# Optimization experiments

Hardware: AMD Instinct MI355X
Metric: run time of the kernel (lower is better)

## Reference

```python
import jax, jax.numpy as jnp
import numpy as np

B, T, V = 512, 200, 2048
E, H, I, A = 20, 100, 64, 32  # embedding, hidden, intermediate, actions


def setup_inputs() -> dict:
    key = jax.random.key(0)
    ks = jax.random.split(key, 12)
    batch = jax.random.uniform(ks[0], (B, T, V), dtype=jnp.float32)
    lengths = jax.random.randint(ks[1], (B,), 1, T + 1)
    s = 0.05
    W_emb = jax.random.normal(ks[2], (E, V), dtype=jnp.float32) * s
    b_emb = jnp.zeros((E,), jnp.float32)
    W_ih = jax.random.normal(ks[3], (4 * H, E), dtype=jnp.float32) * s
    W_hh = jax.random.normal(ks[4], (4 * H, H), dtype=jnp.float32) * s
    b_ih = jnp.zeros((4 * H,), jnp.float32)
    # torch init sets forget-gate bias (second quarter) to 1.0 in bias_hh
    b_hh = jnp.zeros((4 * H,), jnp.float32).at[H:2 * H].set(1.0)
    W1 = jax.random.normal(ks[5], (I, H), dtype=jnp.float32) * s
    b1 = jnp.zeros((I,), jnp.float32)
    W2 = jax.random.normal(ks[6], (A, I), dtype=jnp.float32) * s
    b2 = jnp.zeros((A,), jnp.float32)
    h0 = jnp.zeros((B, H), jnp.float32)
    c0 = jnp.zeros((B, H), jnp.float32)
    return {"batch": batch, "lengths": lengths, "W_emb": W_emb, "b_emb": b_emb,
            "W_ih": W_ih, "W_hh": W_hh, "b_ih": b_ih, "b_hh": b_hh,
            "W1": W1, "b1": b1, "W2": W2, "b2": b2, "h0": h0, "c0": c0}


def reference(batch, lengths, W_emb, b_emb, W_ih, W_hh, b_ih, b_hh,
              W1, b1, W2, b2, h0, c0):
    # Embedding via Linear: [B,T,V] @ [V,E] -> [B,T,E]
    emb = jnp.einsum('btv,ev->bte', batch, W_emb) + b_emb
    # Precompute input contribution to all gates: [B,T,4H]
    xg = jnp.einsum('bte,ge->btg', emb, W_ih) + b_ih + b_hh

    def step(carry, xg_t):
        h, c = carry
        gates = xg_t + h @ W_hh.T  # [B,4H]
        i, f, g, o = jnp.split(gates, 4, axis=-1)  # torch gate order i,f,g,o
        c = jax.nn.sigmoid(f) * c + jax.nn.sigmoid(i) * jnp.tanh(g)
        h = jax.nn.sigmoid(o) * jnp.tanh(c)
        return (h, c), h

    _, ys = jax.lax.scan(step, (h0, c0), jnp.swapaxes(xg, 0, 1))  # ys: [T,B,H]
    nb = batch.shape[0]
    h_final = ys[lengths - 1, jnp.arange(nb)]  # [B,H] output at last valid step
    inter = jax.nn.relu(h_final @ W1.T + b1)
    actions = inter @ W2.T + b2
    return actions
```

## Files before the change

### kernel.cpp

```cpp
#include <hip/hip_runtime.h>

#define BB 512
#define TT 200
#define VV 2048
#define EE 20
#define HH 100
#define G4 400
#define II 64
#define AA 32
#define NT 25
#define NCHUNK 64

typedef _Float16 half8 __attribute__((ext_vector_type(8)));
typedef float    f32x4 __attribute__((ext_vector_type(4)));

#define WS_BF_OFF    1024
#define WS_WIHF_OFF  (WS_BF_OFF + 32768)
#define WS_WHHF_OFF  (WS_WIHF_OFF + 6400)
#define WS_BIASC_OFF (WS_WHHF_OFF + 25600)
#define WS_EMB_OFF   (WS_BIASC_OFF + 400)
#define WS_XG_OFF    (WS_EMB_OFF + 2048000)

__global__ __launch_bounds__(512) void k0_prep(
    const int* __restrict__ lengths, const float* __restrict__ W_emb,
    const float* __restrict__ W_ih, const float* __restrict__ W_hh,
    const float* __restrict__ b_ih, const float* __restrict__ b_hh,
    int* __restrict__ off, _Float16* __restrict__ Bfrag,
    _Float16* __restrict__ Wihf, _Float16* __restrict__ Whhf,
    float* __restrict__ biasc)
{
    if (blockIdx.x == 0) {
        __shared__ int s[BB];
        int tid = threadIdx.x;
        s[tid] = lengths[tid];
        __syncthreads();
        for (int d = 1; d < BB; d <<= 1) {
            int v = (tid >= d) ? s[tid - d] : 0;
            __syncthreads();
            if (tid >= d) s[tid] += v;
            __syncthreads();
        }
        off[tid + 1] = s[tid];
        if (tid == 0) off[0] = 0;
        return;
    }
    int F = (blockIdx.x - 1) * 512 + threadIdx.x;
    if (F < 65536) {
        int e = F & 7, l = (F >> 3) & 63, nn = (F >> 9) & 1, c = F >> 10;
        int k = c * 32 + (l >> 4) * 8 + e;
        int col = nn * 16 + (l & 15);
        float v = (col < EE) ? W_emb[(size_t)col * VV + k] : 0.f;
        Bfrag[F] = (_Float16)v;
        return;
    }
    F -= 65536;
    if (F < 12800) {
        int e = F & 7, l = (F >> 3) & 63, nt = F >> 9;
        int rp = nt * 16 + (l & 15);
        int j = rp >> 2, g = rp & 3;
        int k = 8 * (l >> 4) + e;
        float v = (k < EE) ? W_ih[(size_t)(g * HH + j) * EE + k] : 0.f;
        Wihf[F] = (_Float16)v;
        return;
    }
    F -= 12800;
    if (F < 51200) {
        int e = F & 7, l = (F >> 3) & 63, c = (F >> 9) & 3, m = F >> 11;
        int rp = m * 16 + (l & 15);
        int j = rp >> 2, g = rp & 3;
        int k = 32 * c + 8 * (l >> 4) + e;
        float v = (k < HH) ? W_hh[(size_t)(g * HH + j) * HH + k] : 0.f;
        Whhf[F] = (_Float16)v;
        return;
    }
    F -= 51200;
    if (F < 400) {
        int j = F >> 2, g = F & 3;
        biasc[F] = b_ih[g * HH + j] + b_hh[g * HH + j];
    }
}

__global__ __launch_bounds__(256) void k1_embed(
    const float* __restrict__ batch, const int* __restrict__ off,
    const _Float16* __restrict__ Bfrag, const float* __restrict__ b_emb,
    float* __restrict__ emb)
{
    const int Nv = off[BB];
    if (blockIdx.x * 64 >= Nv) return;

    const int lane  = threadIdx.x & 63;
    const int wid   = threadIdx.x >> 6;
    const int rbase = blockIdx.x * 64 + wid * 16;

    int lrow = rbase + (lane & 15);
    int lr = (lrow < Nv) ? lrow : (Nv - 1);
    int lo = 0, hi = BB;
    while (lo + 1 < hi) {
        int mid = (lo + hi) >> 1;
        if (off[mid] <= lr) lo = mid; else hi = mid;
    }
    const int lroff = lo * TT + (lr - off[lo]);

    const float* __restrict__ aptr = batch + (size_t)lroff * VV + ((lane >> 4) * 8);
    const half8* __restrict__ bptr = reinterpret_cast<const half8*>(Bfrag) + lane;

    f32x4 acc0 = {0.f, 0.f, 0.f, 0.f};
    f32x4 acc1 = {0.f, 0.f, 0.f, 0.f};

#pragma unroll 4
    for (int c = 0; c < NCHUNK; ++c) {
        float4 a0 = *reinterpret_cast<const float4*>(aptr + c * 32);
        float4 a1 = *reinterpret_cast<const float4*>(aptr + c * 32 + 4);
        half8 b0 = bptr[(c * 2 + 0) * 64];
        half8 b1 = bptr[(c * 2 + 1) * 64];
        half8 av;
        av[0] = (_Float16)a0.x; av[1] = (_Float16)a0.y;
        av[2] = (_Float16)a0.z; av[3] = (_Float16)a0.w;
        av[4] = (_Float16)a1.x; av[5] = (_Float16)a1.y;
        av[6] = (_Float16)a1.z; av[7] = (_Float16)a1.w;
        acc0 = __builtin_amdgcn_mfma_f32_16x16x32_f16(av, b0, acc0, 0, 0, 0);
        acc1 = __builtin_amdgcn_mfma_f32_16x16x32_f16(av, b1, acc1, 0, 0, 0);
    }

    const int col0 = lane & 15;
    const float bias0 = b_emb[col0];
    const float bias1 = (col0 < 4) ? b_emb[16 + col0] : 0.f;
#pragma unroll
    for (int r = 0; r < 4; ++r) {
        int srow = rbase + (lane >> 4) * 4 + r;
        if (srow < Nv) {
            emb[(size_t)srow * EE + col0] = acc0[r] + bias0;
            if (col0 < 4)
                emb[(size_t)srow * EE + 16 + col0] = acc1[r] + bias1;
        }
    }
}

__global__ __launch_bounds__(256, 2) void k1_xg(
    const float* __restrict__ emb, const int* __restrict__ off,
    const _Float16* __restrict__ Wihf, const float* __restrict__ biasc,
    float* __restrict__ xg)
{
    __shared__ __align__(16) uint4 wl[NT * 64];
    __shared__ float bl[G4];

    const int tid = threadIdx.x;
    const int Nv = off[BB];
    for (int i = tid; i < NT * 64; i += 256) wl[i] = reinterpret_cast<const uint4*>(Wihf)[i];
    for (int i = tid; i < G4; i += 256) bl[i] = biasc[i];
    __syncthreads();

    const int lane = tid & 63, wid = tid >> 6;
    const int T = blockIdx.x * 4 + wid;
    if (T * 16 >= Nv) return;

    const int lr = min(T * 16 + (lane & 15), Nv - 1);
    const int kb = (lane >> 4) * 8;
    const float* ap = emb + (size_t)lr * EE;
    float4 p0 = make_float4(0.f, 0.f, 0.f, 0.f), p1 = p0;
    if (kb < EE)     p0 = *reinterpret_cast<const float4*>(ap + kb);
    if (kb + 4 < EE) p1 = *reinterpret_cast<const float4*>(ap + kb + 4);
    half8 av;
    av[0] = (_Float16)p0.x; av[1] = (_Float16)p0.y;
    av[2] = (_Float16)p0.z; av[3] = (_Float16)p0.w;
    av[4] = (_Float16)p1.x; av[5] = (_Float16)p1.y;
    av[6] = (_Float16)p1.z; av[7] = (_Float16)p1.w;

    const int rbase = T * 16 + 4 * (lane >> 4);
    const int cl = lane & 15;
#pragma unroll
    for (int nt = 0; nt < NT; ++nt) {
        half8 bf = *reinterpret_cast<const half8*>(&wl[nt * 64 + lane]);
        f32x4 a = {0.f, 0.f, 0.f, 0.f};
        a = __builtin_amdgcn_mfma_f32_16x16x32_f16(av, bf, a, 0, 0, 0);
        float bias = bl[nt * 16 + cl];
#pragma unroll
        for (int r = 0; r < 4; ++r) {
            if (rbase + r < Nv)
                xg[(size_t)(rbase + r) * G4 + nt * 16 + cl] = a[r] + bias;
        }
    }
}

__device__ __forceinline__ float fast_sig(float x) { return 1.f / (1.f + __expf(-x)); }
__device__ __forceinline__ float fast_tanh(float x) { return 2.f * fast_sig(2.f * x) - 1.f; }

#define STEP(T_, CUR_, XC_, XN_)  do {                                                        \
    uint4 rb0_ = *reinterpret_cast<const uint4*>(&bfrag[CUR_][0][lane][0]);                   \
    uint4 rb1_ = *reinterpret_cast<const uint4*>(&bfrag[CUR_][1][lane][0]);                   \
    uint4 rb2_ = *reinterpret_cast<const uint4*>(&bfrag[CUR_][2][lane][0]);                   \
    uint4 rb3_ = *reinterpret_cast<const uint4*>(&bfrag[CUR_][3][lane][0]);                   \
    _Pragma("unroll")                                                                         \
    for (int it = 0; it < 4; ++it) if (it < ntile)                                            \
        XN_[it] = *reinterpret_cast<const float4*>(xg + rowbase + (size_t)((T_) + 1) * G4 + xgoff[it]); \
    _Pragma("unroll")                                                                         \
    for (int it = 0; it < 4; ++it) if (it < ntile) {                                          \
        f32x4 acc = __builtin_bit_cast(f32x4, XC_[it]);                                       \
        acc = __builtin_amdgcn_mfma_f32_16x16x32_f16(af[it][0], __builtin_bit_cast(half8, rb0_), acc, 0, 0, 0); \
        acc = __builtin_amdgcn_mfma_f32_16x16x32_f16(af[it][1], __builtin_bit_cast(half8, rb1_), acc, 0, 0, 0); \
        acc = __builtin_amdgcn_mfma_f32_16x16x32_f16(af[it][2], __builtin_bit_cast(half8, rb2_), acc, 0, 0, 0); \
        acc = __builtin_amdgcn_mfma_f32_16x16x32_f16(af[it][3], __builtin_bit_cast(half8, rb3_), acc, 0, 0, 0); \
        float gi = fast_sig(acc[0]);                                                          \
        float gf = fast_sig(acc[1]);                                                          \
        float gg = fast_tanh(acc[2]);                                                         \
        float go = fast_sig(acc[3]);                                                          \
        cst[it] = gf * cst[it] + gi * gg;                                                     \
        float hv = go * fast_tanh(cst[it]);                                                   \
        int j_ = jidx[it];                                                                    \
        if ((T_) == len_n - 1) hfin[n][j_] = hv;                                              \
        int kk_ = j_ & 31;                                                                    \
        _Float16* hp_ = (_Float16*)&bfrag[(CUR_) ^ 1][j_ >> 5][((kk_ >> 3) << 4) | n][(kk_ & 7) >> 1]; \
        hp_[kk_ & 1] = (_Float16)hv;                                                          \
    }                                                                                         \
    __syncthreads();                                                                          \
} while (0)

__global__ __launch_bounds__(512, 2) void k2_lstm(
    const float* __restrict__ xg, const int* __restrict__ lengths,
    const int* __restrict__ off, const _Float16* __restrict__ Whhf,
    const float* __restrict__ W1, const float* __restrict__ b1,
    const float* __restrict__ W2, const float* __restrict__ b2,
    const float* __restrict__ h0, const float* __restrict__ c0,
    float* __restrict__ out)
{
    __shared__ __align__(16) unsigned int bfrag[2][4][64][4];
    __shared__ float hfin[16][HH];
    __shared__ float inter[16][II];
    __shared__ int len_s[16], off_s[16];

    const int tid  = threadIdx.x;
    const int lane = tid & 63;
    const int w    = tid >> 6;
    const int b0   = blockIdx.x * 16;
    const int n    = lane & 15, rg = lane >> 4;

    if (tid < 16) {
        len_s[tid] = lengths[b0 + tid];
        off_s[tid] = off[b0 + tid];
    }
    for (int i = tid; i < 2 * 4 * 64 * 4; i += 512) (&bfrag[0][0][0][0])[i] = 0u;
    __syncthreads();

    int tmax = 0;
#pragma unroll
    for (int k = 0; k < 16; ++k) tmax = max(tmax, len_s[k]);

    const int ntile = (w == 7) ? 4 : 3;
    const int m0    = (w < 7) ? 3 * w : 21;
    const int len_n = len_s[n];
    const size_t rowbase = (size_t)off_s[n] * G4;

    half8 af[4][4];
    float cst[4];
    int   jidx[4], xgoff[4];
    float4 xgA[4], xgB[4];
#pragma unroll
    for (int it = 0; it < 4; ++it) if (it < ntile) {
        const int m = m0 + it;
#pragma unroll
        for (int c = 0; c < 4; ++c)
            af[it][c] = reinterpret_cast<const half8*>(Whhf)[((m * 4 + c) * 64) + lane];
        const int j = 4 * m + rg;
        jidx[it]  = j;
        xgoff[it] = 16 * m + 4 * rg;
        cst[it] = c0[(size_t)(b0 + n) * HH + j];
        float hv = h0[(size_t)(b0 + n) * HH + j];
        int kk = j & 31;
        _Float16* hp = (_Float16*)&bfrag[0][j >> 5][((kk >> 3) << 4) | n][(kk & 7) >> 1];
        hp[kk & 1] = (_Float16)hv;
        xgA[it] = *reinterpret_cast<const float4*>(xg + rowbase + xgoff[it]);
    }
    __syncthreads();

    for (int t = 0; t < tmax; t += 2) {
        STEP(t, 0, xgA, xgB);
        if (t + 1 < tmax) STEP(t + 1, 1, xgB, xgA);
    }

    for (int o = tid; o < 16 * II; o += 512) {
        int nn = o >> 6, i = o & 63;
        float a = b1[i];
        const float* w1r = W1 + i * HH;
        const float* hr  = &hfin[nn][0];
#pragma unroll
        for (int k = 0; k < HH; k += 4) {
            a += w1r[k] * hr[k] + w1r[k + 1] * hr[k + 1]
               + w1r[k + 2] * hr[k + 2] + w1r[k + 3] * hr[k + 3];
        }
        inter[nn][i] = fmaxf(a, 0.f);
    }
    __syncthreads();
    for (int o = tid; o < 16 * AA; o += 512) {
        int nn = o >> 5, ai = o & 31;
        float a = b2[ai];
        const float* w2r = W2 + ai * II;
#pragma unroll
        for (int k = 0; k < II; ++k) a += w2r[k] * inter[nn][k];
        out[(size_t)(b0 + nn) * AA + ai] = a;
    }
}

extern "C" void kernel_launch(void* const* d_in, const int* in_sizes, int n_in,
                              void* d_out, int out_size, void* d_ws, size_t ws_size,
                              hipStream_t stream) {
    const float* batch  = (const float*)d_in[0];
    const int*   lengths= (const int*)  d_in[1];
    const float* W_emb  = (const float*)d_in[2];
    const float* b_emb  = (const float*)d_in[3];
    const float* W_ih   = (const float*)d_in[4];
    const float* W_hh   = (const float*)d_in[5];
    const float* b_ih   = (const float*)d_in[6];
    const float* b_hh   = (const float*)d_in[7];
    const float* W1     = (const float*)d_in[8];
    const float* b1     = (const float*)d_in[9];
    const float* W2     = (const float*)d_in[10];
    const float* b2     = (const float*)d_in[11];
    const float* h0     = (const float*)d_in[12];
    const float* c0     = (const float*)d_in[13];
    float* out = (float*)d_out;

    int*       off   = (int*)d_ws;
    float*     wsf   = (float*)d_ws;
    _Float16*  Bfrag = (_Float16*)(wsf + WS_BF_OFF);
    _Float16*  Wihf  = (_Float16*)(wsf + WS_WIHF_OFF);
    _Float16*  Whhf  = (_Float16*)(wsf + WS_WHHF_OFF);
    float*     biasc = wsf + WS_BIASC_OFF;
    float*     emb   = wsf + WS_EMB_OFF;
    float*     xg    = wsf + WS_XG_OFF;

    k0_prep<<<255, 512, 0, stream>>>(lengths, W_emb, W_ih, W_hh, b_ih, b_hh,
                                     off, Bfrag, Wihf, Whhf, biasc);
    k1_embed<<<(BB * TT + 63) / 64, 256, 0, stream>>>(batch, off, Bfrag, b_emb, emb);
    k1_xg<<<(BB * TT / 16 + 3) / 4, 256, 0, stream>>>(emb, off, Wihf, biasc, xg);
    k2_lstm<<<BB / 16, 512, 0, stream>>>(xg, lengths, off, Whhf,
                                         W1, b1, W2, b2, h0, c0, out);
}
```

Measured before the change: 432.4 us.

## Fuse input-gate projection into LSTM recurrence and stage embeddings in shared memory

Removes the separate xg kernel and its [N,400] float intermediate. The LSTM kernel now stages fp16 embedding chunks of 16 timesteps in double-buffered shared memory and does one extra MFMA per tile for W_ih·x plus bias. This cuts global traffic and a launch, but adds MFMA work and periodic staging inside the serial recurrence loop.

```diff
diff --git a/kernel.cpp b/kernel.cpp
--- a/kernel.cpp
+++ b/kernel.cpp
@@ -19,7 +19,6 @@
 #define WS_WHHF_OFF  (WS_WIHF_OFF + 6400)
 #define WS_BIASC_OFF (WS_WHHF_OFF + 25600)
 #define WS_EMB_OFF   (WS_BIASC_OFF + 400)
-#define WS_XG_OFF    (WS_EMB_OFF + 2048000)
 
 __global__ __launch_bounds__(512) void k0_prep(
     const int* __restrict__ lengths, const float* __restrict__ W_emb,
@@ -136,66 +135,41 @@
     }
 }
 
-__global__ __launch_bounds__(256, 2) void k1_xg(
-    const float* __restrict__ emb, const int* __restrict__ off,
-    const _Float16* __restrict__ Wihf, const float* __restrict__ biasc,
-    float* __restrict__ xg)
-{
-    __shared__ __align__(16) uint4 wl[NT * 64];
-    __shared__ float bl[G4];
-
-    const int tid = threadIdx.x;
-    const int Nv = off[BB];
-    for (int i = tid; i < NT * 64; i += 256) wl[i] = reinterpret_cast<const uint4*>(Wihf)[i];
-    for (int i = tid; i < G4; i += 256) bl[i] = biasc[i];
-    __syncthreads();
-
-    const int lane = tid & 63, wid = tid >> 6;
-    const int T = blockIdx.x * 4 + wid;
-    if (T * 16 >= Nv) return;
-
-    const int lr = min(T * 16 + (lane & 15), Nv - 1);
-    const int kb = (lane >> 4) * 8;
-    const float* ap = emb + (size_t)lr * EE;
-    float4 p0 = make_float4(0.f, 0.f, 0.f, 0.f), p1 = p0;
-    if (kb < EE)     p0 = *reinterpret_cast<const float4*>(ap + kb);
-    if (kb + 4 < EE) p1 = *reinterpret_cast<const float4*>(ap + kb + 4);
-    half8 av;
-    av[0] = (_Float16)p0.x; av[1] = (_Float16)p0.y;
-    av[2] = (_Float16)p0.z; av[3] = (_Float16)p0.w;
-    av[4] = (_Float16)p1.x; av[5] = (_Float16)p1.y;
-    av[6] = (_Float16)p1.z; av[7] = (_Float16)p1.w;
-
-    const int rbase = T * 16 + 4 * (lane >> 4);
-    const int cl = lane & 15;
-#pragma unroll
-    for (int nt = 0; nt < NT; ++nt) {
-        half8 bf = *reinterpret_cast<const half8*>(&wl[nt * 64 + lane]);
-        f32x4 a = {0.f, 0.f, 0.f, 0.f};
-        a = __builtin_amdgcn_mfma_f32_16x16x32_f16(av, bf, a, 0, 0, 0);
-        float bias = bl[nt * 16 + cl];
-#pragma unroll
-        for (int r = 0; r < 4; ++r) {
-            if (rbase + r < Nv)
-                xg[(size_t)(rbase + r) * G4 + nt * 16 + cl] = a[r] + bias;
-        }
-    }
-}
-
 __device__ __forceinline__ float fast_sig(float x) { return 1.f / (1.f + __expf(-x)); }
 __device__ __forceinline__ float fast_tanh(float x) { return 2.f * fast_sig(2.f * x) - 1.f; }
-
-#define STEP(T_, CUR_, XC_, XN_)  do {                                                        \
+__device__ __forceinline__ unsigned int packh2(float f0, float f1) {
+    unsigned short u0 = __builtin_bit_cast(unsigned short, (_Float16)f0);
+    unsigned short u1 = __builtin_bit_cast(unsigned short, (_Float16)f1);
+    return ((unsigned int)u1 << 16) | u0;
+}
+
+#define STAGE_CHUNK(DST_, CB_)  do {                                                          \
+    for (int i_ = tid; i_ < 1280; i_ += 512) {                                                \
+        int t16_ = i_ / 80, rem_ = i_ - t16_ * 80;                                            \
+        int nn_ = rem_ / 5, q_ = rem_ - nn_ * 5;                                              \
+        int ts_ = (CB_) + t16_;                                                               \
+        int lm1_ = len_s[nn_] - 1;                                                            \
+        ts_ = (ts_ < lm1_) ? ts_ : lm1_;                                                      \
+        float4 v_ = *reinterpret_cast<const float4*>(                                         \
+            emb + (size_t)(off_s[nn_] + ts_) * EE + q_ * 4);                                  \
+        uint2 p_;                                                                             \
+        p_.x = packh2(v_.x, v_.y);                                                            \
+        p_.y = packh2(v_.z, v_.w);                                                            \
+        *reinterpret_cast<uint2*>(&estage[DST_][t16_][nn_][q_ * 4]) = p_;                     \
+    }                                                                                         \
+} while (0)
+
+#define STEP(T_, CUR_)  do {                                                                  \
+    const int sb_ = ((T_) >> 4) & 1;                                                          \
+    uint4 xb_  = *reinterpret_cast<const uint4*>(&estage[sb_][(T_) & 15][n][(lane >> 4) * 8]);\
     uint4 rb0_ = *reinterpret_cast<const uint4*>(&bfrag[CUR_][0][lane][0]);                   \
     uint4 rb1_ = *reinterpret_cast<const uint4*>(&bfrag[CUR_][1][lane][0]);                   \
     uint4 rb2_ = *reinterpret_cast<const uint4*>(&bfrag[CUR_][2][lane][0]);                   \
     uint4 rb3_ = *reinterpret_cast<const uint4*>(&bfrag[CUR_][3][lane][0]);                   \
     _Pragma("unroll")                                                                         \
-    for (int it = 0; it < 4; ++it) if (it < ntile)                                            \
-        XN_[it] = *reinterpret_cast<const float4*>(xg + rowbase + (size_t)((T_) + 1) * G4 + xgoff[it]); \
-    _Pragma("unroll")                                                                         \
     for (int it = 0; it < 4; ++it) if (it < ntile) {                                          \
-        f32x4 acc = __builtin_bit_cast(f32x4, XC_[it]);                                       \
+        f32x4 acc = biasf[it];                                                                \
+        acc = __builtin_amdgcn_mfma_f32_16x16x32_f16(wif[it], __builtin_bit_cast(half8, xb_), acc, 0, 0, 0); \
         acc = __builtin_amdgcn_mfma_f32_16x16x32_f16(af[it][0], __builtin_bit_cast(half8, rb0_), acc, 0, 0, 0); \
         acc = __builtin_amdgcn_mfma_f32_16x16x32_f16(af[it][1], __builtin_bit_cast(half8, rb1_), acc, 0, 0, 0); \
         acc = __builtin_amdgcn_mfma_f32_16x16x32_f16(af[it][2], __builtin_bit_cast(half8, rb2_), acc, 0, 0, 0); \
@@ -212,18 +186,23 @@
         _Float16* hp_ = (_Float16*)&bfrag[(CUR_) ^ 1][j_ >> 5][((kk_ >> 3) << 4) | n][(kk_ & 7) >> 1]; \
         hp_[kk_ & 1] = (_Float16)hv;                                                          \
     }                                                                                         \
+    if (((T_) & 15) == 0 && (T_) + 16 < tmax) {                                               \
+        STAGE_CHUNK(sb_ ^ 1, (T_) + 16);                                                      \
+    }                                                                                         \
     __syncthreads();                                                                          \
 } while (0)
 
 __global__ __launch_bounds__(512, 2) void k2_lstm(
-    const float* __restrict__ xg, const int* __restrict__ lengths,
+    const float* __restrict__ emb, const int* __restrict__ lengths,
     const int* __restrict__ off, const _Float16* __restrict__ Whhf,
+    const _Float16* __restrict__ Wihf, const float* __restrict__ biasc,
     const float* __restrict__ W1, const float* __restrict__ b1,
     const float* __restrict__ W2, const float* __restrict__ b2,
     const float* __restrict__ h0, const float* __restrict__ c0,
     float* __restrict__ out)
 {
     __shared__ __align__(16) unsigned int bfrag[2][4][64][4];
+    __shared__ __align__(16) _Float16 estage[2][16][16][40];
     __shared__ float hfin[16][HH];
     __shared__ float inter[16][II];
     __shared__ int len_s[16], off_s[16];
@@ -239,6 +218,8 @@
         off_s[tid] = off[b0 + tid];
     }
     for (int i = tid; i < 2 * 4 * 64 * 4; i += 512) (&bfrag[0][0][0][0])[i] = 0u;
+    for (int i = tid; i < 2 * 16 * 16 * 40 / 2; i += 512)
+        reinterpret_cast<unsigned int*>(&estage[0][0][0][0])[i] = 0u;
     __syncthreads();
 
     int tmax = 0;
@@ -248,34 +229,36 @@
     const int ntile = (w == 7) ? 4 : 3;
     const int m0    = (w < 7) ? 3 * w : 21;
     const int len_n = len_s[n];
-    const size_t rowbase = (size_t)off_s[n] * G4;
 
     half8 af[4][4];
+    half8 wif[4];
+    f32x4 biasf[4];
     float cst[4];
-    int   jidx[4], xgoff[4];
-    float4 xgA[4], xgB[4];
+    int   jidx[4];
 #pragma unroll
     for (int it = 0; it < 4; ++it) if (it < ntile) {
         const int m = m0 + it;
 #pragma unroll
         for (int c = 0; c < 4; ++c)
             af[it][c] = reinterpret_cast<const half8*>(Whhf)[((m * 4 + c) * 64) + lane];
+        wif[it]   = reinterpret_cast<const half8*>(Wihf)[m * 64 + lane];
+        biasf[it] = *reinterpret_cast<const f32x4*>(biasc + 16 * m + 4 * rg);
         const int j = 4 * m + rg;
-        jidx[it]  = j;
-        xgoff[it] = 16 * m + 4 * rg;
+        jidx[it] = j;
         cst[it] = c0[(size_t)(b0 + n) * HH + j];
         float hv = h0[(size_t)(b0 + n) * HH + j];
         int kk = j & 31;
         _Float16* hp = (_Float16*)&bfrag[0][j >> 5][((kk >> 3) << 4) | n][(kk & 7) >> 1];
         hp[kk & 1] = (_Float16)hv;
-        xgA[it] = *reinterpret_cast<const float4*>(xg + rowbase + xgoff[it]);
-    }
+    }
+    STAGE_CHUNK(0, 0);
     __syncthreads();
 
     for (int t = 0; t < tmax; t += 2) {
-        STEP(t, 0, xgA, xgB);
-        if (t + 1 < tmax) STEP(t + 1, 1, xgB, xgA);
-    }
+        STEP(t, 0);
+        if (t + 1 < tmax) STEP(t + 1, 1);
+    }
+    __syncthreads();
 
     for (int o = tid; o < 16 * II; o += 512) {
         int nn = o >> 6, i = o & 63;
@@ -326,12 +309,10 @@
     _Float16*  Whhf  = (_Float16*)(wsf + WS_WHHF_OFF);
     float*     biasc = wsf + WS_BIASC_OFF;
     float*     emb   = wsf + WS_EMB_OFF;
-    float*     xg    = wsf + WS_XG_OFF;
 
     k0_prep<<<255, 512, 0, stream>>>(lengths, W_emb, W_ih, W_hh, b_ih, b_hh,
                                      off, Bfrag, Wihf, Whhf, biasc);
     k1_embed<<<(BB * TT + 63) / 64, 256, 0, stream>>>(batch, off, Bfrag, b_emb, emb);
-    k1_xg<<<(BB * TT / 16 + 3) / 4, 256, 0, stream>>>(emb, off, Wihf, biasc, xg);
-    k2_lstm<<<BB / 16, 512, 0, stream>>>(xg, lengths, off, Whhf,
+    k2_lstm<<<BB / 16, 512, 0, stream>>>(emb, lengths, off, Whhf, Wihf, biasc,
                                          W1, b1, W2, b2, h0, c0, out);
 }
```

Result: faster. 402.7 us (-6.9%).
